# Kernel optimization log

Hardware: AMD Instinct MI355X
Metric: run time of the kernel (lower is better)

Reference implementation:

```python
import jax, jax.numpy as jnp
import numpy as np

N = 40000      # nodes
E = 640000     # edges (avg degree 16)
F_IN = 33      # input residue features (hard-coded in module)
H = 128        # hidden_channels
C_OUT = 3      # output classes (hard-coded)
L = 8          # num_layers
ALPHA = 0.1
THETA = 0.5


def setup_inputs() -> dict:
    key = jax.random.key(0)
    ks = jax.random.split(key, 8)
    x = jax.random.normal(ks[0], (N, F_IN), jnp.float32)
    edge_row = jax.random.randint(ks[1], (E,), 0, N)
    edge_col = jax.random.randint(ks[2], (E,), 0, N)
    edge_weight = jax.random.uniform(ks[3], (E,), jnp.float32)
    # nn.Linear stores weight as [out, in]
    W_in = jax.random.normal(ks[4], (H, F_IN), jnp.float32) * 0.1
    b_in = jnp.zeros((H,), jnp.float32)
    W_out = jax.random.normal(ks[5], (C_OUT, H), jnp.float32) * 0.1
    b_out = jnp.zeros((C_OUT,), jnp.float32)
    # GCN2Conv shared weight1 per layer: [L, H, H]
    W_conv = jax.random.normal(ks[6], (L, H, H), jnp.float32) * (1.0 / np.sqrt(H))
    return dict(x=x, edge_row=edge_row, edge_col=edge_col, edge_weight=edge_weight,
                W_in=W_in, b_in=b_in, W_out=W_out, b_out=b_out, W_conv=W_conv)


def reference(x, edge_row, edge_col, edge_weight, W_in, b_in, W_out, b_out, W_conv):
    # dropout p=0.0 -> identity (also eval mode)
    x0 = jax.nn.relu(x @ W_in.T + b_in)                      # [N, H]
    # GCN2Conv beta_l = log(theta / layer + 1), layer = 1..L
    betas = jnp.log(THETA / jnp.arange(1.0, L + 1.0, dtype=jnp.float32) + 1.0)

    def spmm(h):
        # adj_t @ h : gather source-node features, weight, scatter-add to rows
        return jax.ops.segment_sum(edge_weight[:, None] * h[edge_col], edge_row,
                                   num_segments=N)

    def step(xc, lw):
        W, beta = lw
        # GCN2Conv (shared_weights=True, normalize=False):
        #   xx = (1-alpha)*A@h + alpha*x0 ; out = (1-beta)*xx + beta*(xx@W)
        xx = (1.0 - ALPHA) * spmm(xc) + ALPHA * x0
        out = (1.0 - beta) * xx + beta * (xx @ W)
        return xc + jax.nn.relu(out), None                   # residual in GCN.forward

    x_final, _ = jax.lax.scan(step, x0, (W_conv, betas))
    return x_final @ W_out.T + b_out                          # [N, 3]
```

## Files before the change

### kernel.cpp

```cpp
#include <hip/hip_runtime.h>
#include <hip/hip_bf16.h>
#include <math.h>

#define N_NODES 40000
#define NE      640000
#define FIN     33
#define H       128
#define COUT    3
#define NLAYERS 8
#define ALPHA   0.1f
#define THETA   0.5f
#define CAP     96

#define SB_SCAT 625
#define SB_WPRE 512
#define SB_XIN  2500

typedef __bf16 bf16x8 __attribute__((ext_vector_type(8)));
typedef float  f32x4  __attribute__((ext_vector_type(4)));

__device__ inline unsigned short f2bf(float f) {
    __hip_bfloat16 b = __float2bfloat16(f);
    return *(unsigned short*)&b;
}
__device__ inline float bf2f(unsigned short u) {
    __hip_bfloat16 b = *(__hip_bfloat16*)&u;
    return __bfloat162float(b);
}

__global__ __launch_bounds__(256) void k_setup(
        const int* __restrict__ row, const int* __restrict__ col,
        const float* __restrict__ w, int* __restrict__ cnt,
        unsigned int* __restrict__ bucket,
        const float* __restrict__ Wconv, unsigned short* __restrict__ Wtbf,
        const float* __restrict__ x, const float* __restrict__ Win,
        const float* __restrict__ bin,
        unsigned short* __restrict__ x0bf, unsigned short* __restrict__ hbf) {
    __shared__ float sW[H * FIN];
    __shared__ float sx[16][FIN];
    int b = blockIdx.x, t = threadIdx.x;

    if (b < SB_SCAT) {
        int e0 = (b * 256 + t) * 4;
        int r[4], pos[4];
        unsigned int rec[4];
        #pragma unroll
        for (int i = 0; i < 4; i++) {
            int e = e0 + i;
            r[i] = row[e];
            unsigned int wb = f2bf((1.0f - ALPHA) * w[e]);
            rec[i] = (wb << 16) | (unsigned int)col[e];
        }
        #pragma unroll
        for (int i = 0; i < 4; i++) pos[i] = atomicAdd(&cnt[r[i]], 1);
        #pragma unroll
        for (int i = 0; i < 4; i++) bucket[(size_t)r[i] * CAP + pos[i]] = rec[i];
        return;
    }
    if (b < SB_SCAT + SB_WPRE) {
        int idx = (b - SB_SCAT) * 256 + t;
        int l = idx >> 14;
        int rem = idx & 16383;
        int k = rem >> 7, j = rem & 127;
        float beta = logf(THETA / (float)(l + 1) + 1.0f);
        float v = beta * Wconv[idx];
        if (j == k) v += 1.0f - beta;
        Wtbf[l * 16384 + j * 128 + k] = f2bf(v);
        return;
    }
    {
        int n0 = (b - SB_SCAT - SB_WPRE) * 16;
        for (int i = t; i < H * FIN; i += 256) sW[i] = Win[i];
        for (int i = t; i < 16 * FIN; i += 256)
            sx[i / FIN][i % FIN] = x[(size_t)(n0 + i / FIN) * FIN + (i % FIN)];
        __syncthreads();
        int f = t % H;
        int l0 = t / H;
        float bv = bin[f];
        for (int lo = l0; lo < 16; lo += 2) {
            float acc = bv;
            #pragma unroll
            for (int k = 0; k < FIN; k++) acc += sx[lo][k] * sW[f * FIN + k];
            acc = fmaxf(acc, 0.f);
            size_t idx = (size_t)(n0 + lo) * H + f;
            unsigned short bb = f2bf(acc);
            x0bf[idx] = bb;
            hbf[idx] = bb;
        }
    }
}

__global__ __launch_bounds__(256) void k_spmm(const int* __restrict__ cnt,
                       const unsigned int* __restrict__ bucket,
                       const unsigned short* __restrict__ hbf,
                       const unsigned short* __restrict__ x0bf,
                       unsigned short* __restrict__ xxbf) {
    int wave = (blockIdx.x * blockDim.x + threadIdx.x) >> 6;
    int lane = threadIdx.x & 63;
    if (wave >= N_NODES) return;
    int deg = cnt[wave];
    const unsigned int* ep = bucket + (size_t)wave * CAP;
    int slot = lane >> 4;
    int fid  = lane & 15;

    float acc[8] = {0,0,0,0,0,0,0,0};

    for (int e = 0; e < deg; e += 16) {
        unsigned int u[4];
        uint4 q[4];
        #pragma unroll
        for (int k = 0; k < 4; k++) {
            int ei = e + k * 4 + slot;
            unsigned int uu = ep[ei];
            u[k] = (ei < deg) ? uu : 0u;
        }
        #pragma unroll
        for (int k = 0; k < 4; k++)
            q[k] = *(const uint4*)(hbf + (size_t)(u[k] & 0xffffu) * H + fid * 8);
        #pragma unroll
        for (int k = 0; k < 4; k++) {
            float w = bf2f((unsigned short)(u[k] >> 16));
            acc[0] += w * bf2f((unsigned short)(q[k].x & 0xffffu));
            acc[1] += w * bf2f((unsigned short)(q[k].x >> 16));
            acc[2] += w * bf2f((unsigned short)(q[k].y & 0xffffu));
            acc[3] += w * bf2f((unsigned short)(q[k].y >> 16));
            acc[4] += w * bf2f((unsigned short)(q[k].z & 0xffffu));
            acc[5] += w * bf2f((unsigned short)(q[k].z >> 16));
            acc[6] += w * bf2f((unsigned short)(q[k].w & 0xffffu));
            acc[7] += w * bf2f((unsigned short)(q[k].w >> 16));
        }
    }

    #pragma unroll
    for (int j = 0; j < 8; j++) {
        acc[j] += __shfl_xor(acc[j], 16);
        acc[j] += __shfl_xor(acc[j], 32);
    }

    if (slot == 0) {
        uint4 xq = *(const uint4*)(x0bf + (size_t)wave * H + fid * 8);
        float o0 = acc[0] + ALPHA * bf2f((unsigned short)(xq.x & 0xffffu));
        float o1 = acc[1] + ALPHA * bf2f((unsigned short)(xq.x >> 16));
        float o2 = acc[2] + ALPHA * bf2f((unsigned short)(xq.y & 0xffffu));
        float o3 = acc[3] + ALPHA * bf2f((unsigned short)(xq.y >> 16));
        float o4 = acc[4] + ALPHA * bf2f((unsigned short)(xq.z & 0xffffu));
        float o5 = acc[5] + ALPHA * bf2f((unsigned short)(xq.z >> 16));
        float o6 = acc[6] + ALPHA * bf2f((unsigned short)(xq.w & 0xffffu));
        float o7 = acc[7] + ALPHA * bf2f((unsigned short)(xq.w >> 16));
        uint4 r;
        r.x = (unsigned int)f2bf(o0) | ((unsigned int)f2bf(o1) << 16);
        r.y = (unsigned int)f2bf(o2) | ((unsigned int)f2bf(o3) << 16);
        r.z = (unsigned int)f2bf(o4) | ((unsigned int)f2bf(o5) << 16);
        r.w = (unsigned int)f2bf(o6) | ((unsigned int)f2bf(o7) << 16);
        *(uint4*)(xxbf + (size_t)wave * H + fid * 8) = r;
    }
}

__global__ __launch_bounds__(128) void k_gemm(const unsigned short* __restrict__ xxbf,
                       const unsigned short* __restrict__ Wtbf,
                       unsigned short* __restrict__ hbf,
                       const float* __restrict__ Wout, const float* __restrict__ bout,
                       float* __restrict__ out, int do_out) {
    int t = threadIdx.x;
    int wv = t >> 6, lane = t & 63;
    int quad = lane >> 4, l16 = lane & 15;
    int rbase = blockIdx.x * 32 + wv * 16;

    f32x4 acc[8];
    #pragma unroll
    for (int j = 0; j < 8; j++) acc[j] = (f32x4){0.f, 0.f, 0.f, 0.f};

    #pragma unroll
    for (int k0 = 0; k0 < 4; k0++) {
        bf16x8 av = *(const bf16x8*)(xxbf + (size_t)(rbase + l16) * H + k0 * 32 + quad * 8);
        #pragma unroll
        for (int j = 0; j < 8; j++) {
            bf16x8 bv = *(const bf16x8*)(Wtbf + (size_t)(j * 16 + l16) * H + k0 * 32 + quad * 8);
            acc[j] = __builtin_amdgcn_mfma_f32_16x16x32_bf16(av, bv, acc[j], 0, 0, 0);
        }
    }

    float po[4][3];
    #pragma unroll
    for (int r = 0; r < 4; r++) { po[r][0] = 0.f; po[r][1] = 0.f; po[r][2] = 0.f; }

    #pragma unroll
    for (int j = 0; j < 8; j++) {
        int col = j * 16 + l16;
        float w0 = 0.f, w1 = 0.f, w2 = 0.f;
        if (do_out) { w0 = Wout[col]; w1 = Wout[H + col]; w2 = Wout[2 * H + col]; }
        #pragma unroll
        for (int r = 0; r < 4; r++) {
            int row = rbase + quad * 4 + r;
            size_t idx = (size_t)row * H + col;
            float hv = bf2f(hbf[idx]) + fmaxf(acc[j][r], 0.f);
            hbf[idx] = f2bf(hv);
            po[r][0] += hv * w0; po[r][1] += hv * w1; po[r][2] += hv * w2;
        }
    }

    if (do_out) {
        #pragma unroll
        for (int off = 1; off < 16; off <<= 1) {
            #pragma unroll
            for (int r = 0; r < 4; r++) {
                po[r][0] += __shfl_xor(po[r][0], off);
                po[r][1] += __shfl_xor(po[r][1], off);
                po[r][2] += __shfl_xor(po[r][2], off);
            }
        }
        if (l16 == 0) {
            #pragma unroll
            for (int r = 0; r < 4; r++) {
                int row = rbase + quad * 4 + r;
                out[(size_t)row * 3 + 0] = po[r][0] + bout[0];
                out[(size_t)row * 3 + 1] = po[r][1] + bout[1];
                out[(size_t)row * 3 + 2] = po[r][2] + bout[2];
            }
        }
    }
}

extern "C" void kernel_launch(void* const* d_in, const int* in_sizes, int n_in,
                              void* d_out, int out_size, void* d_ws, size_t ws_size,
                              hipStream_t stream) {
    const float* x     = (const float*)d_in[0];
    const int*   erow  = (const int*)  d_in[1];
    const int*   ecol  = (const int*)  d_in[2];
    const float* ew    = (const float*)d_in[3];
    const float* Win   = (const float*)d_in[4];
    const float* bin   = (const float*)d_in[5];
    const float* Wout  = (const float*)d_in[6];
    const float* bout  = (const float*)d_in[7];
    const float* Wconv = (const float*)d_in[8];
    float* out = (float*)d_out;

    char* ws = (char*)d_ws;
    const size_t NHb = (size_t)N_NODES * H * sizeof(unsigned short);
    unsigned short* xxbf  = (unsigned short*)(ws);
    unsigned short* x0bf  = (unsigned short*)(ws + NHb);
    unsigned short* hbf   = (unsigned short*)(ws + 2 * NHb);
    char* p = ws + 3 * NHb;
    unsigned short* Wtbf  = (unsigned short*)p;  p += 8 * H * H * 2;
    int*  cnt     = (int*) p;  p += 160256;
    unsigned int* bucket = (unsigned int*)p;

    hipMemsetAsync(cnt, 0, (size_t)N_NODES * 4, stream);
    k_setup<<<SB_SCAT + SB_WPRE + SB_XIN, 256, 0, stream>>>(
        erow, ecol, ew, cnt, bucket, Wconv, Wtbf, x, Win, bin, x0bf, hbf);

    for (int l = 0; l < NLAYERS; l++) {
        k_spmm<<<N_NODES / 4,  256, 0, stream>>>(cnt, bucket, hbf, x0bf, xxbf);
        k_gemm<<<N_NODES / 32, 128, 0, stream>>>(xxbf, Wtbf + (size_t)l * H * H,
                                                 hbf, Wout, bout, out,
                                                 (l == NLAYERS - 1) ? 1 : 0);
    }
}
```

Before: 458.2 us.

## Fuse SpMM and GEMM into one per-layer kernel with LDS staging and ping-pong buffers

```diff
diff --git a/kernel.cpp b/kernel.cpp
--- a/kernel.cpp
+++ b/kernel.cpp
@@ -35,7 +35,7 @@
         const float* __restrict__ Wconv, unsigned short* __restrict__ Wtbf,
         const float* __restrict__ x, const float* __restrict__ Win,
         const float* __restrict__ bin,
-        unsigned short* __restrict__ x0bf, unsigned short* __restrict__ hbf) {
+        unsigned short* __restrict__ x0bf) {
     __shared__ float sW[H * FIN];
     __shared__ float sx[16][FIN];
     int b = blockIdx.x, t = threadIdx.x;
@@ -82,140 +82,158 @@
             #pragma unroll
             for (int k = 0; k < FIN; k++) acc += sx[lo][k] * sW[f * FIN + k];
             acc = fmaxf(acc, 0.f);
-            size_t idx = (size_t)(n0 + lo) * H + f;
-            unsigned short bb = f2bf(acc);
-            x0bf[idx] = bb;
-            hbf[idx] = bb;
-        }
-    }
-}
-
-__global__ __launch_bounds__(256) void k_spmm(const int* __restrict__ cnt,
-                       const unsigned int* __restrict__ bucket,
-                       const unsigned short* __restrict__ hbf,
-                       const unsigned short* __restrict__ x0bf,
-                       unsigned short* __restrict__ xxbf) {
-    int wave = (blockIdx.x * blockDim.x + threadIdx.x) >> 6;
-    int lane = threadIdx.x & 63;
-    if (wave >= N_NODES) return;
-    int deg = cnt[wave];
-    const unsigned int* ep = bucket + (size_t)wave * CAP;
-    int slot = lane >> 4;
-    int fid  = lane & 15;
-
-    float acc[8] = {0,0,0,0,0,0,0,0};
-
-    for (int e = 0; e < deg; e += 16) {
-        unsigned int u[4];
-        uint4 q[4];
-        #pragma unroll
-        for (int k = 0; k < 4; k++) {
-            int ei = e + k * 4 + slot;
-            unsigned int uu = ep[ei];
-            u[k] = (ei < deg) ? uu : 0u;
-        }
-        #pragma unroll
-        for (int k = 0; k < 4; k++)
-            q[k] = *(const uint4*)(hbf + (size_t)(u[k] & 0xffffu) * H + fid * 8);
-        #pragma unroll
-        for (int k = 0; k < 4; k++) {
-            float w = bf2f((unsigned short)(u[k] >> 16));
-            acc[0] += w * bf2f((unsigned short)(q[k].x & 0xffffu));
-            acc[1] += w * bf2f((unsigned short)(q[k].x >> 16));
-            acc[2] += w * bf2f((unsigned short)(q[k].y & 0xffffu));
-            acc[3] += w * bf2f((unsigned short)(q[k].y >> 16));
-            acc[4] += w * bf2f((unsigned short)(q[k].z & 0xffffu));
-            acc[5] += w * bf2f((unsigned short)(q[k].z >> 16));
-            acc[6] += w * bf2f((unsigned short)(q[k].w & 0xffffu));
-            acc[7] += w * bf2f((unsigned short)(q[k].w >> 16));
-        }
-    }
-
-    #pragma unroll
-    for (int j = 0; j < 8; j++) {
-        acc[j] += __shfl_xor(acc[j], 16);
-        acc[j] += __shfl_xor(acc[j], 32);
-    }
-
-    if (slot == 0) {
-        uint4 xq = *(const uint4*)(x0bf + (size_t)wave * H + fid * 8);
-        float o0 = acc[0] + ALPHA * bf2f((unsigned short)(xq.x & 0xffffu));
-        float o1 = acc[1] + ALPHA * bf2f((unsigned short)(xq.x >> 16));
-        float o2 = acc[2] + ALPHA * bf2f((unsigned short)(xq.y & 0xffffu));
-        float o3 = acc[3] + ALPHA * bf2f((unsigned short)(xq.y >> 16));
-        float o4 = acc[4] + ALPHA * bf2f((unsigned short)(xq.z & 0xffffu));
-        float o5 = acc[5] + ALPHA * bf2f((unsigned short)(xq.z >> 16));
-        float o6 = acc[6] + ALPHA * bf2f((unsigned short)(xq.w & 0xffffu));
-        float o7 = acc[7] + ALPHA * bf2f((unsigned short)(xq.w >> 16));
-        uint4 r;
-        r.x = (unsigned int)f2bf(o0) | ((unsigned int)f2bf(o1) << 16);
-        r.y = (unsigned int)f2bf(o2) | ((unsigned int)f2bf(o3) << 16);
-        r.z = (unsigned int)f2bf(o4) | ((unsigned int)f2bf(o5) << 16);
-        r.w = (unsigned int)f2bf(o6) | ((unsigned int)f2bf(o7) << 16);
-        *(uint4*)(xxbf + (size_t)wave * H + fid * 8) = r;
-    }
-}
-
-__global__ __launch_bounds__(128) void k_gemm(const unsigned short* __restrict__ xxbf,
-                       const unsigned short* __restrict__ Wtbf,
-                       unsigned short* __restrict__ hbf,
-                       const float* __restrict__ Wout, const float* __restrict__ bout,
-                       float* __restrict__ out, int do_out) {
+            x0bf[(size_t)(n0 + lo) * H + f] = f2bf(acc);
+        }
+    }
+}
+
+__global__ __launch_bounds__(256) void k_layer(
+        const int* __restrict__ cnt, const unsigned int* __restrict__ bucket,
+        const unsigned short* __restrict__ hin,
+        const unsigned short* __restrict__ x0bf,
+        const unsigned short* __restrict__ Wt,
+        unsigned short* __restrict__ hout,
+        const float* __restrict__ Wout, const float* __restrict__ bout,
+        float* __restrict__ out, int do_out) {
+    __shared__ __align__(16) char smem[16896];
+
     int t = threadIdx.x;
     int wv = t >> 6, lane = t & 63;
+    int rbase = blockIdx.x * 32;
+
+    {
+        int slot = lane >> 4;
+        int fid  = lane & 15;
+        for (int i = 0; i < 8; i++) {
+            int rloc = wv * 8 + i;
+            int row  = rbase + rloc;
+            int deg  = cnt[row];
+            const unsigned int* ep = bucket + (size_t)row * CAP;
+            float acc[8] = {0,0,0,0,0,0,0,0};
+
+            for (int e = 0; e < deg; e += 16) {
+                unsigned int u[4];
+                uint4 q[4];
+                #pragma unroll
+                for (int k = 0; k < 4; k++) {
+                    int ei = e + k * 4 + slot;
+                    unsigned int uu = ep[ei];
+                    u[k] = (ei < deg) ? uu : 0u;
+                }
+                #pragma unroll
+                for (int k = 0; k < 4; k++)
+                    q[k] = *(const uint4*)(hin + (size_t)(u[k] & 0xffffu) * H + fid * 8);
+                #pragma unroll
+                for (int k = 0; k < 4; k++) {
+                    float w = bf2f((unsigned short)(u[k] >> 16));
+                    acc[0] += w * bf2f((unsigned short)(q[k].x & 0xffffu));
+                    acc[1] += w * bf2f((unsigned short)(q[k].x >> 16));
+                    acc[2] += w * bf2f((unsigned short)(q[k].y & 0xffffu));
+                    acc[3] += w * bf2f((unsigned short)(q[k].y >> 16));
+                    acc[4] += w * bf2f((unsigned short)(q[k].z & 0xffffu));
+                    acc[5] += w * bf2f((unsigned short)(q[k].z >> 16));
+                    acc[6] += w * bf2f((unsigned short)(q[k].w & 0xffffu));
+                    acc[7] += w * bf2f((unsigned short)(q[k].w >> 16));
+                }
+            }
+            #pragma unroll
+            for (int j = 0; j < 8; j++) {
+                acc[j] += __shfl_xor(acc[j], 16);
+                acc[j] += __shfl_xor(acc[j], 32);
+            }
+            if (slot == 0) {
+                uint4 xq = *(const uint4*)(x0bf + (size_t)row * H + fid * 8);
+                float o0 = acc[0] + ALPHA * bf2f((unsigned short)(xq.x & 0xffffu));
+                float o1 = acc[1] + ALPHA * bf2f((unsigned short)(xq.x >> 16));
+                float o2 = acc[2] + ALPHA * bf2f((unsigned short)(xq.y & 0xffffu));
+                float o3 = acc[3] + ALPHA * bf2f((unsigned short)(xq.y >> 16));
+                float o4 = acc[4] + ALPHA * bf2f((unsigned short)(xq.z & 0xffffu));
+                float o5 = acc[5] + ALPHA * bf2f((unsigned short)(xq.z >> 16));
+                float o6 = acc[6] + ALPHA * bf2f((unsigned short)(xq.w & 0xffffu));
+                float o7 = acc[7] + ALPHA * bf2f((unsigned short)(xq.w >> 16));
+                uint4 r;
+                r.x = (unsigned int)f2bf(o0) | ((unsigned int)f2bf(o1) << 16);
+                r.y = (unsigned int)f2bf(o2) | ((unsigned int)f2bf(o3) << 16);
+                r.z = (unsigned int)f2bf(o4) | ((unsigned int)f2bf(o5) << 16);
+                r.w = (unsigned int)f2bf(o6) | ((unsigned int)f2bf(o7) << 16);
+                *(uint4*)(smem + (size_t)rloc * 272 + fid * 16) = r;
+            }
+        }
+    }
+    __syncthreads();
+
     int quad = lane >> 4, l16 = lane & 15;
-    int rbase = blockIdx.x * 32 + wv * 16;
-
-    f32x4 acc[8];
-    #pragma unroll
-    for (int j = 0; j < 8; j++) acc[j] = (f32x4){0.f, 0.f, 0.f, 0.f};
+    int rh = (wv >> 1) * 16;
+    int ch = (wv & 1) * 64;
+    f32x4 acc2[4];
+    #pragma unroll
+    for (int j = 0; j < 4; j++) acc2[j] = (f32x4){0.f, 0.f, 0.f, 0.f};
 
     #pragma unroll
     for (int k0 = 0; k0 < 4; k0++) {
-        bf16x8 av = *(const bf16x8*)(xxbf + (size_t)(rbase + l16) * H + k0 * 32 + quad * 8);
-        #pragma unroll
-        for (int j = 0; j < 8; j++) {
-            bf16x8 bv = *(const bf16x8*)(Wtbf + (size_t)(j * 16 + l16) * H + k0 * 32 + quad * 8);
-            acc[j] = __builtin_amdgcn_mfma_f32_16x16x32_bf16(av, bv, acc[j], 0, 0, 0);
-        }
-    }
-
-    float po[4][3];
-    #pragma unroll
-    for (int r = 0; r < 4; r++) { po[r][0] = 0.f; po[r][1] = 0.f; po[r][2] = 0.f; }
-
-    #pragma unroll
-    for (int j = 0; j < 8; j++) {
-        int col = j * 16 + l16;
-        float w0 = 0.f, w1 = 0.f, w2 = 0.f;
-        if (do_out) { w0 = Wout[col]; w1 = Wout[H + col]; w2 = Wout[2 * H + col]; }
-        #pragma unroll
-        for (int r = 0; r < 4; r++) {
-            int row = rbase + quad * 4 + r;
-            size_t idx = (size_t)row * H + col;
-            float hv = bf2f(hbf[idx]) + fmaxf(acc[j][r], 0.f);
-            hbf[idx] = f2bf(hv);
-            po[r][0] += hv * w0; po[r][1] += hv * w1; po[r][2] += hv * w2;
-        }
-    }
-
-    if (do_out) {
-        #pragma unroll
-        for (int off = 1; off < 16; off <<= 1) {
-            #pragma unroll
-            for (int r = 0; r < 4; r++) {
-                po[r][0] += __shfl_xor(po[r][0], off);
-                po[r][1] += __shfl_xor(po[r][1], off);
-                po[r][2] += __shfl_xor(po[r][2], off);
-            }
-        }
-        if (l16 == 0) {
-            #pragma unroll
-            for (int r = 0; r < 4; r++) {
-                int row = rbase + quad * 4 + r;
-                out[(size_t)row * 3 + 0] = po[r][0] + bout[0];
-                out[(size_t)row * 3 + 1] = po[r][1] + bout[1];
-                out[(size_t)row * 3 + 2] = po[r][2] + bout[2];
+        bf16x8 av = *(const bf16x8*)(smem + (size_t)(rh + l16) * 272 + k0 * 64 + quad * 16);
+        #pragma unroll
+        for (int j = 0; j < 4; j++) {
+            bf16x8 bv = *(const bf16x8*)(Wt + (size_t)(ch + j * 16 + l16) * H + k0 * 32 + quad * 8);
+            acc2[j] = __builtin_amdgcn_mfma_f32_16x16x32_bf16(av, bv, acc2[j], 0, 0, 0);
+        }
+    }
+    __syncthreads();
+
+    float* facc = (float*)smem;
+    #pragma unroll
+    for (int j = 0; j < 4; j++) {
+        #pragma unroll
+        for (int r = 0; r < 4; r++)
+            facc[(rh + quad * 4 + r) * 132 + ch + j * 16 + l16] = acc2[j][r];
+    }
+    __syncthreads();
+
+    int cb = (t & 15) * 8;
+    #pragma unroll
+    for (int p = 0; p < 2; p++) {
+        int rloc = p * 16 + (t >> 4);
+        int row  = rbase + rloc;
+        const float* fr = facc + rloc * 132 + cb;
+        f32x4 a0 = *(const f32x4*)fr;
+        f32x4 a1 = *(const f32x4*)(fr + 4);
+        uint4 hq = *(const uint4*)(hin + (size_t)row * H + cb);
+        float hv[8];
+        hv[0] = bf2f((unsigned short)(hq.x & 0xffffu)) + fmaxf(a0[0], 0.f);
+        hv[1] = bf2f((unsigned short)(hq.x >> 16))     + fmaxf(a0[1], 0.f);
+        hv[2] = bf2f((unsigned short)(hq.y & 0xffffu)) + fmaxf(a0[2], 0.f);
+        hv[3] = bf2f((unsigned short)(hq.y >> 16))     + fmaxf(a0[3], 0.f);
+        hv[4] = bf2f((unsigned short)(hq.z & 0xffffu)) + fmaxf(a1[0], 0.f);
+        hv[5] = bf2f((unsigned short)(hq.z >> 16))     + fmaxf(a1[1], 0.f);
+        hv[6] = bf2f((unsigned short)(hq.w & 0xffffu)) + fmaxf(a1[2], 0.f);
+        hv[7] = bf2f((unsigned short)(hq.w >> 16))     + fmaxf(a1[3], 0.f);
+
+        if (!do_out) {
+            uint4 rr;
+            rr.x = (unsigned int)f2bf(hv[0]) | ((unsigned int)f2bf(hv[1]) << 16);
+            rr.y = (unsigned int)f2bf(hv[2]) | ((unsigned int)f2bf(hv[3]) << 16);
+            rr.z = (unsigned int)f2bf(hv[4]) | ((unsigned int)f2bf(hv[5]) << 16);
+            rr.w = (unsigned int)f2bf(hv[6]) | ((unsigned int)f2bf(hv[7]) << 16);
+            *(uint4*)(hout + (size_t)row * H + cb) = rr;
+        } else {
+            float p0 = 0.f, p1 = 0.f, p2 = 0.f;
+            #pragma unroll
+            for (int i2 = 0; i2 < 8; i2++) {
+                float h = hv[i2];
+                p0 += h * Wout[cb + i2];
+                p1 += h * Wout[H + cb + i2];
+                p2 += h * Wout[2 * H + cb + i2];
+            }
+            #pragma unroll
+            for (int off = 1; off < 16; off <<= 1) {
+                p0 += __shfl_xor(p0, off);
+                p1 += __shfl_xor(p1, off);
+                p2 += __shfl_xor(p2, off);
+            }
+            if ((t & 15) == 0) {
+                out[(size_t)row * 3 + 0] = p0 + bout[0];
+                out[(size_t)row * 3 + 1] = p1 + bout[1];
+                out[(size_t)row * 3 + 2] = p2 + bout[2];
             }
         }
     }
@@ -237,9 +255,9 @@
 
     char* ws = (char*)d_ws;
     const size_t NHb = (size_t)N_NODES * H * sizeof(unsigned short);
-    unsigned short* xxbf  = (unsigned short*)(ws);
-    unsigned short* x0bf  = (unsigned short*)(ws + NHb);
-    unsigned short* hbf   = (unsigned short*)(ws + 2 * NHb);
+    unsigned short* x0bf  = (unsigned short*)(ws);
+    unsigned short* bufA  = (unsigned short*)(ws + NHb);
+    unsigned short* bufB  = (unsigned short*)(ws + 2 * NHb);
     char* p = ws + 3 * NHb;
     unsigned short* Wtbf  = (unsigned short*)p;  p += 8 * H * H * 2;
     int*  cnt     = (int*) p;  p += 160256;
@@ -247,12 +265,13 @@
 
     hipMemsetAsync(cnt, 0, (size_t)N_NODES * 4, stream);
     k_setup<<<SB_SCAT + SB_WPRE + SB_XIN, 256, 0, stream>>>(
-        erow, ecol, ew, cnt, bucket, Wconv, Wtbf, x, Win, bin, x0bf, hbf);
+        erow, ecol, ew, cnt, bucket, Wconv, Wtbf, x, Win, bin, x0bf);
 
     for (int l = 0; l < NLAYERS; l++) {
-        k_spmm<<<N_NODES / 4,  256, 0, stream>>>(cnt, bucket, hbf, x0bf, xxbf);
-        k_gemm<<<N_NODES / 32, 128, 0, stream>>>(xxbf, Wtbf + (size_t)l * H * H,
-                                                 hbf, Wout, bout, out,
-                                                 (l == NLAYERS - 1) ? 1 : 0);
-    }
-}
+        const unsigned short* hin = (l == 0) ? x0bf : ((l & 1) ? bufA : bufB);
+        unsigned short* hout = (l & 1) ? bufB : bufA;
+        k_layer<<<N_NODES / 32, 256, 0, stream>>>(
+            cnt, bucket, hin, x0bf, Wtbf + (size_t)l * H * H,
+            hout, Wout, bout, out, (l == NLAYERS - 1) ? 1 : 0);
+    }
+}
```

Result: faster. 392.2 us (-14.4%).
